# Kernel optimization log

Hardware: AMD Instinct MI355X
Metric: run time of the kernel (lower is better)

## Reference

```python
import jax, jax.numpy as jnp
import numpy as np

B, I, O, H = 1024, 128, 128, 5  # batch, input_size, output_size, hidden_size


def setup_inputs() -> dict:
    key = jax.random.key(0)
    ks = jax.random.split(key, 7)
    s = 0.3  # modest init scale, like torch default Linear init range
    return {
        "x": jax.random.normal(ks[0], (B, I), dtype=jnp.float32),
        # stacked per-edge MLP params: one tiny MLP per (output_node, input_node) edge
        "W1": jax.random.normal(ks[1], (O, I, H), dtype=jnp.float32) * s,  # Linear(1,H).weight
        "B1": jax.random.normal(ks[2], (O, I, H), dtype=jnp.float32) * s,
        "W2": jax.random.normal(ks[3], (O, I, H, H), dtype=jnp.float32) * s,  # Linear(H,H).weight (out,in)
        "B2": jax.random.normal(ks[4], (O, I, H), dtype=jnp.float32) * s,
        "W3": jax.random.normal(ks[5], (O, I, H), dtype=jnp.float32) * s,  # Linear(H,1).weight
        "B3": jax.random.normal(ks[6], (O, I), dtype=jnp.float32) * s,
    }


def reference(x, W1, B1, W2, B2, W3, B3):
    # Per-edge MLP, vectorized over all O*I edges at once.
    lrelu = lambda t: jax.nn.leaky_relu(t, negative_slope=0.01)  # torch LeakyReLU default
    # layer 1: scalar input -> H. [B,O,I,H]
    h1 = lrelu(x[:, None, :, None] * W1 + B1)
    # layer 2: H -> H per edge. torch Linear: y = h @ W.T, W is (out,in) -> contract 'in' axis
    h2 = lrelu(jnp.einsum("boih,oikh->boik", h1, W2) + B2)
    # layer 3: H -> scalar per edge, then sum over input nodes j
    y_edge = jnp.einsum("boih,oih->boi", h2, W3) + B3  # [B,O,I]
    return y_edge.sum(axis=2)  # [B,O]
```

## Files before the change

kernel.cpp:

```cpp
#include <hip/hip_runtime.h>

#define Bsz 1024
#define Isz 128
#define Osz 128
#define Hsz 5
#define GB 32
#define NG (Bsz / GB)
#define UF 4

template <int CTRL>
__device__ __forceinline__ float dpp_add(float s) {
    int t = __builtin_amdgcn_update_dpp(0, __builtin_bit_cast(int, s),
                                        CTRL, 0xf, 0xf, true);
    return s + __builtin_bit_cast(float, t);
}
__device__ __forceinline__ float wave_sum64_lane63(float s) {
    s = dpp_add<0xB1>(s);
    s = dpp_add<0x4E>(s);
    s = dpp_add<0x141>(s);
    s = dpp_add<0x140>(s);
    s = dpp_add<0x142>(s);
    s = dpp_add<0x143>(s);
    return s;
}

__global__ __launch_bounds__(256, 6)
void kan_kernel(const float* __restrict__ x,
                const float* __restrict__ W1, const float* __restrict__ B1,
                const float* __restrict__ W2, const float* __restrict__ B2,
                const float* __restrict__ W3, const float* __restrict__ B3,
                float* __restrict__ out) {
    __shared__ float xs[GB * Isz];
    __shared__ float partial[4 * GB];

    const int tid = threadIdx.x;
    const int ob  = blockIdx.x & 63;
    const int g   = blockIdx.x >> 6;
    const int b0  = g * GB;
    const int w   = tid >> 6;
    const int l   = tid & 63;
    const int o   = 2 * ob + (w >> 1);
    const int i   = 64 * (w & 1) + l;
    const int e   = o * Isz + i;

    {
        const float4* xg = (const float4*)(x + (size_t)b0 * Isz);
        float4* xs4 = (float4*)xs;
        #pragma unroll
        for (int j = 0; j < (GB * Isz / 4) / 256; ++j)
            xs4[tid + 256 * j] = xg[tid + 256 * j];
    }

    float w1[Hsz], b1[Hsz], w2[Hsz * Hsz], b2[Hsz], w3[Hsz];
    #pragma unroll
    for (int h = 0; h < Hsz; ++h) {
        w1[h] = W1[(size_t)e * Hsz + h];
        b1[h] = B1[(size_t)e * Hsz + h];
        b2[h] = B2[(size_t)e * Hsz + h];
        w3[h] = W3[(size_t)e * Hsz + h];
    }
    #pragma unroll
    for (int j = 0; j < Hsz * Hsz; ++j) w2[j] = W2[(size_t)e * Hsz * Hsz + j];

    const float s3w = wave_sum64_lane63(B3[e]);
    const float s3  = __builtin_bit_cast(float,
        __builtin_amdgcn_readlane(__builtin_bit_cast(int, s3w), 63));

    __syncthreads();

    float res = 0.0f;

    #pragma unroll
    for (int bl = 0; bl < GB; bl += UF) {
        float y[UF];
        #pragma unroll
        for (int u = 0; u < UF; ++u) {
            const float a = xs[(bl + u) * Isz + i];

            float h1[Hsz];
            #pragma unroll
            for (int h = 0; h < Hsz; ++h) {
                float v = fmaf(a, w1[h], b1[h]);
                h1[h] = fmaxf(v, 0.01f * v);
            }
            float yy = 0.0f;
            #pragma unroll
            for (int k = 0; k < Hsz; ++k) {
                float s = b2[k];
                #pragma unroll
                for (int h = 0; h < Hsz; ++h)
                    s = fmaf(h1[h], w2[k * Hsz + h], s);
                s = fmaxf(s, 0.01f * s);
                yy = fmaf(s, w3[k], yy);
            }
            y[u] = yy;
        }

        #pragma unroll
        for (int u = 0; u < UF; ++u) {
            const float s = wave_sum64_lane63(y[u]);
            const float tot = __builtin_bit_cast(float,
                __builtin_amdgcn_readlane(__builtin_bit_cast(int, s), 63));
            if (l == bl + u) res = tot;
        }
    }

    if (l < GB) partial[w * GB + l] = res + s3;
    __syncthreads();

    if (tid < 2 * GB) {
        const int bl = tid & (GB - 1);
        const int oo = tid >> 5;
        const float v = partial[(2 * oo) * GB + bl] + partial[(2 * oo + 1) * GB + bl];
        out[(size_t)(b0 + bl) * Osz + (2 * ob + oo)] = v;
    }
}

extern "C" void kernel_launch(void* const* d_in, const int* in_sizes, int n_in,
                              void* d_out, int out_size, void* d_ws, size_t ws_size,
                              hipStream_t stream) {
    const float* x  = (const float*)d_in[0];
    const float* W1 = (const float*)d_in[1];
    const float* B1 = (const float*)d_in[2];
    const float* W2 = (const float*)d_in[3];
    const float* B2 = (const float*)d_in[4];
    const float* W3 = (const float*)d_in[5];
    const float* B3 = (const float*)d_in[6];
    float* out = (float*)d_out;

    const dim3 grid((Osz / 2) * NG);
    kan_kernel<<<grid, dim3(256), 0, stream>>>(x, W1, B1, W2, B2, W3, B3, out);
}
```

Measured before the change: 89.57 us.

## Repack per-edge params into contiguous records and map lanes to batch rows

Adds a prepass kernel that packs each edge's W1/B1/W2/B2/W3/B3 into one 48-float record in workspace. The main kernel now puts batch rows on lanes and loops over 32 input nodes per wave. Because every lane in a wave reads the same record, parameter loads become wave-uniform (scalar/broadcast) and the per-batch DPP wave reductions go away. The cost is an extra launch and a full parameter copy on every call, plus x held per lane in 32 registers.

```diff
diff --git a/kernel.cpp b/kernel.cpp
--- a/kernel.cpp
+++ b/kernel.cpp
@@ -4,115 +4,86 @@
 #define Isz 128
 #define Osz 128
 #define Hsz 5
-#define GB 32
-#define NG (Bsz / GB)
-#define UF 4
+#define Esz (Osz * Isz)
+#define REC 48
 
-template <int CTRL>
-__device__ __forceinline__ float dpp_add(float s) {
-    int t = __builtin_amdgcn_update_dpp(0, __builtin_bit_cast(int, s),
-                                        CTRL, 0xf, 0xf, true);
-    return s + __builtin_bit_cast(float, t);
-}
-__device__ __forceinline__ float wave_sum64_lane63(float s) {
-    s = dpp_add<0xB1>(s);
-    s = dpp_add<0x4E>(s);
-    s = dpp_add<0x141>(s);
-    s = dpp_add<0x140>(s);
-    s = dpp_add<0x142>(s);
-    s = dpp_add<0x143>(s);
-    return s;
+__global__ __launch_bounds__(256)
+void relayout_params(const float* __restrict__ W1, const float* __restrict__ B1,
+                     const float* __restrict__ W2, const float* __restrict__ B2,
+                     const float* __restrict__ W3, const float* __restrict__ B3,
+                     float* __restrict__ pt2) {
+    const int idx = blockIdx.x * 256 + threadIdx.x;
+    const unsigned e = (unsigned)idx / REC;
+    const int j = idx - (int)e * REC;
+    float v = 0.0f;
+    if (j < 5)        v = W1[e * 5 + j];
+    else if (j < 10)  v = B1[e * 5 + (j - 5)];
+    else if (j < 35)  v = W2[e * 25 + (j - 10)];
+    else if (j < 40)  v = B2[e * 5 + (j - 35)];
+    else if (j < 45)  v = W3[e * 5 + (j - 40)];
+    else if (j == 45) v = B3[e];
+    pt2[idx] = v;
 }
 
-__global__ __launch_bounds__(256, 6)
+__global__ __launch_bounds__(256, 4)
 void kan_kernel(const float* __restrict__ x,
-                const float* __restrict__ W1, const float* __restrict__ B1,
-                const float* __restrict__ W2, const float* __restrict__ B2,
-                const float* __restrict__ W3, const float* __restrict__ B3,
+                const float* __restrict__ pt2,
                 float* __restrict__ out) {
-    __shared__ float xs[GB * Isz];
-    __shared__ float partial[4 * GB];
+    __shared__ float partial[4][64];
 
     const int tid = threadIdx.x;
-    const int ob  = blockIdx.x & 63;
-    const int g   = blockIdx.x >> 6;
-    const int b0  = g * GB;
-    const int w   = tid >> 6;
+    const int o   = blockIdx.x & (Osz - 1);
+    const int bg  = blockIdx.x >> 7;
+    const int b0  = bg * 64;
     const int l   = tid & 63;
-    const int o   = 2 * ob + (w >> 1);
-    const int i   = 64 * (w & 1) + l;
-    const int e   = o * Isz + i;
+    const int wu  = __builtin_amdgcn_readfirstlane(tid >> 6);
 
+    float xr[32];
     {
-        const float4* xg = (const float4*)(x + (size_t)b0 * Isz);
-        float4* xs4 = (float4*)xs;
+        const float4* xrow = (const float4*)(x + (size_t)(b0 + l) * Isz + 32 * wu);
         #pragma unroll
-        for (int j = 0; j < (GB * Isz / 4) / 256; ++j)
-            xs4[tid + 256 * j] = xg[tid + 256 * j];
-    }
-
-    float w1[Hsz], b1[Hsz], w2[Hsz * Hsz], b2[Hsz], w3[Hsz];
-    #pragma unroll
-    for (int h = 0; h < Hsz; ++h) {
-        w1[h] = W1[(size_t)e * Hsz + h];
-        b1[h] = B1[(size_t)e * Hsz + h];
-        b2[h] = B2[(size_t)e * Hsz + h];
-        w3[h] = W3[(size_t)e * Hsz + h];
-    }
-    #pragma unroll
-    for (int j = 0; j < Hsz * Hsz; ++j) w2[j] = W2[(size_t)e * Hsz * Hsz + j];
-
-    const float s3w = wave_sum64_lane63(B3[e]);
-    const float s3  = __builtin_bit_cast(float,
-        __builtin_amdgcn_readlane(__builtin_bit_cast(int, s3w), 63));
-
-    __syncthreads();
-
-    float res = 0.0f;
-
-    #pragma unroll
-    for (int bl = 0; bl < GB; bl += UF) {
-        float y[UF];
-        #pragma unroll
-        for (int u = 0; u < UF; ++u) {
-            const float a = xs[(bl + u) * Isz + i];
-
-            float h1[Hsz];
-            #pragma unroll
-            for (int h = 0; h < Hsz; ++h) {
-                float v = fmaf(a, w1[h], b1[h]);
-                h1[h] = fmaxf(v, 0.01f * v);
-            }
-            float yy = 0.0f;
-            #pragma unroll
-            for (int k = 0; k < Hsz; ++k) {
-                float s = b2[k];
-                #pragma unroll
-                for (int h = 0; h < Hsz; ++h)
-                    s = fmaf(h1[h], w2[k * Hsz + h], s);
-                s = fmaxf(s, 0.01f * s);
-                yy = fmaf(s, w3[k], yy);
-            }
-            y[u] = yy;
-        }
-
-        #pragma unroll
-        for (int u = 0; u < UF; ++u) {
-            const float s = wave_sum64_lane63(y[u]);
-            const float tot = __builtin_bit_cast(float,
-                __builtin_amdgcn_readlane(__builtin_bit_cast(int, s), 63));
-            if (l == bl + u) res = tot;
+        for (int c = 0; c < 8; ++c) {
+            const float4 v = xrow[c];
+            xr[4 * c + 0] = v.x; xr[4 * c + 1] = v.y;
+            xr[4 * c + 2] = v.z; xr[4 * c + 3] = v.w;
         }
     }
 
-    if (l < GB) partial[w * GB + l] = res + s3;
+    const float* __restrict__ pbase = pt2 + (size_t)(o * Isz + 32 * wu) * REC;
+
+    float acc = 0.0f;
+
+    #pragma unroll
+    for (int ii = 0; ii < 32; ++ii) {
+        const float* __restrict__ p = pbase + ii * REC;
+        const float a = xr[ii];
+
+        float h1[Hsz];
+        #pragma unroll
+        for (int h = 0; h < Hsz; ++h) {
+            const float v = fmaf(a, p[h], p[5 + h]);
+            h1[h] = fmaxf(v, 0.01f * v);
+        }
+        float yy = p[45];
+        #pragma unroll
+        for (int k = 0; k < Hsz; ++k) {
+            float s = p[35 + k];
+            #pragma unroll
+            for (int h = 0; h < Hsz; ++h)
+                s = fmaf(h1[h], p[10 + k * Hsz + h], s);
+            s = fmaxf(s, 0.01f * s);
+            yy = fmaf(s, p[40 + k], yy);
+        }
+        acc += yy;
+    }
+
+    partial[wu][l] = acc;
     __syncthreads();
 
-    if (tid < 2 * GB) {
-        const int bl = tid & (GB - 1);
-        const int oo = tid >> 5;
-        const float v = partial[(2 * oo) * GB + bl] + partial[(2 * oo + 1) * GB + bl];
-        out[(size_t)(b0 + bl) * Osz + (2 * ob + oo)] = v;
+    if (tid < 64) {
+        const float v = partial[0][tid] + partial[1][tid]
+                      + partial[2][tid] + partial[3][tid];
+        out[(size_t)(b0 + tid) * Osz + o] = v;
     }
 }
 
@@ -127,7 +98,10 @@
     const float* W3 = (const float*)d_in[5];
     const float* B3 = (const float*)d_in[6];
     float* out = (float*)d_out;
+    float* pt2 = (float*)d_ws;
 
-    const dim3 grid((Osz / 2) * NG);
-    kan_kernel<<<grid, dim3(256), 0, stream>>>(x, W1, B1, W2, B2, W3, B3, out);
+    relayout_params<<<dim3(Esz * REC / 256), dim3(256), 0, stream>>>(
+        W1, B1, W2, B2, W3, B3, pt2);
+
+    kan_kernel<<<dim3(Osz * (Bsz / 64)), dim3(256), 0, stream>>>(x, pt2, out);
 }
```

Measured after the change: 99.07 us. +10.6%, slower.
